# Optimization experiments

Hardware: AMD Instinct MI355X
Metric: run time of the kernel (lower is better)

## Reference

```python
import jax, jax.numpy as jnp
import numpy as np

# Conv config (matches init_kwargs): 3x3 conv, 256->256, stride 1, pad 1
KH, KW = 3, 3
STRIDE = (1, 1)
PAD = ((1, 1), (1, 1))


def setup_inputs() -> dict:
    key = jax.random.key(0)
    k1, k2, k3 = jax.random.split(key, 3)
    x = jax.random.normal(k1, (32, 256, 56, 56), dtype=jnp.float32)
    # linear.weight = conv.weight.view(C_out, C_in*kH*kW) -> [256, 2304]
    weight = jax.random.normal(k2, (256, 256 * KH * KW), dtype=jnp.float32) * 0.02
    bias = jax.random.normal(k3, (256,), dtype=jnp.float32)
    return {"x": x, "weight": weight, "bias": bias}


def reference(x, weight, bias):
    # im2col (same layout/order as F.unfold: feature dim = C * kH * kW, c-major)
    # patches: [N, C*kH*kW, H_out, W_out]
    patches = jax.lax.conv_general_dilated_patches(
        x, filter_shape=(KH, KW), window_strides=STRIDE, padding=PAD
    )
    # dense GEMM over the unfolded feature dim (the nn.Linear)
    y = jnp.einsum("nkhw,ok->nohw", patches, weight)
    y = y + bias[None, :, None, None]
    return y
```

## Files before the change

kernel.cpp:

```cpp
#include <hip/hip_runtime.h>
#include <hip/hip_bf16.h>

typedef short bf16x8 __attribute__((ext_vector_type(8)));
typedef float f32x4  __attribute__((ext_vector_type(4)));
typedef unsigned int uint4v __attribute__((ext_vector_type(4)));

#define HWHW   3136
#define ROWSH  40
#define ROWBYTES 80

__device__ __forceinline__ unsigned short f2bf(float f) {
    unsigned int u = __float_as_uint(f);
    u += 0x7fffu + ((u >> 16) & 1u);
    return (unsigned short)(u >> 16);
}

__global__ void wprep(const float* __restrict__ w, unsigned short* __restrict__ wt) {
    int idx = blockIdx.x * blockDim.x + threadIdx.x;
    int e    = idx & 7;
    int lane = (idx >> 3) & 63;
    int om   = (idx >> 9) & 15;
    int c8   = (idx >> 13) & 7;
    int t    = idx >> 16;
    int o = om * 16 + (lane & 15);
    int c = c8 * 32 + (lane >> 4) * 8 + e;
    wt[idx] = f2bf(w[o * 2304 + c * 9 + t]);
}

__global__ void xprep(const float* __restrict__ x, unsigned short* __restrict__ xt) {
    const int hp = blockIdx.x;
    const int c8 = blockIdx.y;
    const int n  = blockIdx.z;
    const int t  = threadIdx.x;
    const int wp  = t >> 2;
    const int ccq = t & 3;
    const int h = hp - 1, w = wp - 1;
    const bool ok = (h >= 0) && (h < 56) && (w >= 0) && (w < 56);
    const int sp = ok ? (h * 56 + w) : 0;
    const float* xr = x + ((size_t)n * 256 + c8 * 32 + ccq * 8) * HWHW + sp;
    uint4v d;
#pragma unroll
    for (int p = 0; p < 4; ++p) {
        float f0 = ok ? xr[(size_t)(2 * p) * HWHW] : 0.0f;
        float f1 = ok ? xr[(size_t)(2 * p + 1) * HWHW] : 0.0f;
        d[p] = (unsigned)f2bf(f0) | ((unsigned)f2bf(f1) << 16);
    }
    *(uint4v*)(xt + ((((size_t)n * 8 + c8) * 58 + hp) * 2048) + wp * 32 + ccq * 8) = d;
}

__global__ __launch_bounds__(256, 2)
void conv_main(const unsigned short* __restrict__ xt, const unsigned short* __restrict__ wt,
               const float* __restrict__ bias, float* __restrict__ out) {
    __shared__ __align__(16) short xs[2][6 * 64 * ROWSH];

    const int bx = blockIdx.x;
    const int hb = bx >> 1;
    const int bm = bx & 1;
    const int n  = blockIdx.y;
    const int h0 = hb * 4;

    const int tid  = threadIdx.x;
    const int lane = tid & 63;
    const int wv   = tid >> 6;
    const int wm   = wv & 1;
    const int ng   = wv >> 1;
    const int g    = lane >> 4;
    const int lcol = lane & 15;

    int bboff[7][3];
#pragma unroll
    for (int f = 0; f < 7; ++f) {
        int j = ng * 112 + f * 16 + lcol;
        int r = j / 56, wc = j % 56;
#pragma unroll
        for (int kw = 0; kw < 3; ++kw) {
            int ww  = wc + kw;
            int bit = (ww >> 3) & 1;
            bboff[f][kw] = (r * 64 + ww) * ROWBYTES + 16 * (g ^ bit);
        }
    }

    const int sg  = tid & 3;
    const int swp = (tid >> 2) & 63;
    const int swb = swp * ROWBYTES + 16 * (sg ^ ((swp >> 3) & 1));

    const unsigned short* wl = wt + (size_t)lane * 8;
    const int obase = bm * 8 + wm * 4;

    f32x4 acc[4][7];
#pragma unroll
    for (int m = 0; m < 4; ++m)
#pragma unroll
        for (int f = 0; f < 7; ++f) acc[m][f] = (f32x4){0.f, 0.f, 0.f, 0.f};

    bf16x8 sv[6];
    auto s_load = [&](int c8) {
        const unsigned short* p = xt + (((size_t)n * 8 + c8) * 58 + h0) * 2048 + swp * 32 + sg * 8;
#pragma unroll
        for (int r = 0; r < 6; ++r) sv[r] = *(const bf16x8*)(p + (size_t)r * 2048);
    };
    auto s_write = [&](int buf) {
        char* d = (char*)&xs[buf][0] + swb;
#pragma unroll
        for (int r = 0; r < 6; ++r)
            *(bf16x8*)(d + r * 64 * ROWBYTES) = sv[r];
    };

    s_load(0);
    s_write(0);
    __syncthreads();

    for (int c8 = 0; c8 < 8; ++c8) {
        const bool more = c8 < 7;
        const char* xb = (const char*)&xs[c8 & 1][0];

        bf16x8 a0[4], a1[4];
#pragma unroll
        for (int m = 0; m < 4; ++m)
            a0[m] = *(const bf16x8*)(wl + (size_t)((c8 * 16) + obase + m) * 512);

#pragma unroll
        for (int t = 0; t < 9; ++t) {
            bf16x8* ac = (t & 1) ? a1 : a0;
            bf16x8* an = (t & 1) ? a0 : a1;
            if (t < 8) {
#pragma unroll
                for (int m = 0; m < 4; ++m)
                    an[m] = *(const bf16x8*)(wl + (size_t)((((t + 1) * 8 + c8) * 16) + obase + m) * 512);
            }
            const int kh = t / 3, kw = t % 3;
            const int dt = kh * 64 * ROWBYTES;
#pragma unroll
            for (int f = 0; f < 7; ++f) {
                bf16x8 b = *(const bf16x8*)(xb + bboff[f][kw] + dt);
#pragma unroll
                for (int m = 0; m < 4; ++m)
                    acc[m][f] = __builtin_amdgcn_mfma_f32_16x16x32_bf16(ac[m], b, acc[m][f], 0, 0, 0);
            }
            if (t == 4 && more) s_load(c8 + 1);
        }

        if (more) s_write((c8 + 1) & 1);
        __syncthreads();
    }

#pragma unroll
    for (int m = 0; m < 4; ++m) {
#pragma unroll
        for (int q = 0; q < 4; ++q) {
            int o = bm * 128 + wm * 64 + m * 16 + 4 * g + q;
            float bs = bias[o];
            float* yo = out + ((size_t)n * 256 + o) * HWHW + hb * 224;
#pragma unroll
            for (int f = 0; f < 7; ++f) {
                int j = ng * 112 + f * 16 + lcol;
                yo[j] = acc[m][f][q] + bs;
            }
        }
    }
}

__global__ __launch_bounds__(512, 2)
void conv_fallback(const float* __restrict__ x, const unsigned short* __restrict__ wt,
                   const float* __restrict__ bias, float* __restrict__ out) {
    __shared__ short xs[2][348 * 40];
    const int hb = blockIdx.x, n = blockIdx.y, h0 = hb * 4;
    const int tid = threadIdx.x, lane = tid & 63, wv = tid >> 6;
    const int wm = wv & 3, ng = wv >> 2, g = lane >> 4, lcol = lane & 15;
    int bbase[7];
#pragma unroll
    for (int f = 0; f < 7; ++f) {
        int j = ng * 112 + f * 16 + lcol;
        bbase[f] = ((j / 56) * 58 + (j % 56)) * 40 + 8 * g;
    }
    const int cpair = tid >> 5, col0 = tid & 31;
    const float* xn = x + (size_t)n * 256 * HWHW;
    float sv0[6][2], sv1[6][2];
    f32x4 acc[4][7];
#pragma unroll
    for (int m = 0; m < 4; ++m)
#pragma unroll
        for (int f = 0; f < 7; ++f) acc[m][f] = (f32x4){0.f, 0.f, 0.f, 0.f};
    const unsigned short* wl = wt + (size_t)lane * 8;
    auto stage_load = [&](int c8) {
        const float* xc0 = xn + (size_t)(c8 * 32 + 2 * cpair) * HWHW;
        const float* xc1 = xc0 + HWHW;
#pragma unroll
        for (int r = 0; r < 6; ++r) {
            int hh = h0 - 1 + r;
            bool rok = (hh >= 0) & (hh < 56);
#pragma unroll
            for (int ci = 0; ci < 2; ++ci) {
                int col = col0 + 32 * ci, ww = col - 1;
                bool ok = rok & (col < 58) & (ww >= 0) & (ww < 56);
                int off = hh * 56 + ww;
                sv0[r][ci] = ok ? xc0[off] : 0.0f;
                sv1[r][ci] = ok ? xc1[off] : 0.0f;
            }
        }
    };
    auto stage_write = [&](int buf) {
#pragma unroll
        for (int r = 0; r < 6; ++r)
#pragma unroll
            for (int ci = 0; ci < 2; ++ci) {
                int col = col0 + 32 * ci;
                if (col < 58) {
                    unsigned int p = (unsigned int)f2bf(sv0[r][ci]) |
                                     ((unsigned int)f2bf(sv1[r][ci]) << 16);
                    *(unsigned int*)&xs[buf][(r * 58 + col) * 40 + 2 * cpair] = p;
                }
            }
    };
    stage_load(0); stage_write(0);
    __syncthreads();
    for (int c8 = 0; c8 < 8; ++c8) {
        if (c8 < 7) stage_load(c8 + 1);
        const short* xb = &xs[c8 & 1][0];
        bf16x8 a0[4], a1[4];
#pragma unroll
        for (int m = 0; m < 4; ++m)
            a0[m] = *(const bf16x8*)(wl + (size_t)((c8 * 16) + 4 * wm + m) * 512);
#pragma unroll
        for (int t = 0; t < 9; ++t) {
            bf16x8* ac = (t & 1) ? a1 : a0;
            bf16x8* an = (t & 1) ? a0 : a1;
            if (t < 8) {
#pragma unroll
                for (int m = 0; m < 4; ++m)
                    an[m] = *(const bf16x8*)(wl + (size_t)((((t + 1) * 8 + c8) * 16) + 4 * wm + m) * 512);
            }
            const int dt = ((t / 3) * 58 + (t % 3)) * 40;
#pragma unroll
            for (int f = 0; f < 7; ++f) {
                bf16x8 b = *(const bf16x8*)&xb[bbase[f] + dt];
#pragma unroll
                for (int m = 0; m < 4; ++m)
                    acc[m][f] = __builtin_amdgcn_mfma_f32_16x16x32_bf16(ac[m], b, acc[m][f], 0, 0, 0);
            }
        }
        if (c8 < 7) stage_write((c8 + 1) & 1);
        __syncthreads();
    }
#pragma unroll
    for (int m = 0; m < 4; ++m) {
#pragma unroll
        for (int q = 0; q < 4; ++q) {
            int o = 64 * wm + 16 * m + 4 * g + q;
            float bs = bias[o];
            float* yo = out + ((size_t)n * 256 + o) * HWHW + h0 * 56;
#pragma unroll
            for (int f = 0; f < 7; ++f) {
                int j = ng * 112 + f * 16 + lcol;
                yo[j] = acc[m][f][q] + bs;
            }
        }
    }
}

extern "C" void kernel_launch(void* const* d_in, const int* in_sizes, int n_in,
                              void* d_out, int out_size, void* d_ws, size_t ws_size,
                              hipStream_t stream) {
    const float* x    = (const float*)d_in[0];
    const float* w    = (const float*)d_in[1];
    const float* bias = (const float*)d_in[2];
    float* out        = (float*)d_out;
    unsigned short* wt = (unsigned short*)d_ws;
    unsigned short* xtp = (unsigned short*)((char*)d_ws + 1179648);

    wprep<<<2304, 256, 0, stream>>>(w, wt);
    if (ws_size >= (size_t)1179648 + 60817408) {
        xprep<<<dim3(58, 8, 32), 256, 0, stream>>>(x, xtp);
        conv_main<<<dim3(28, 32), 256, 0, stream>>>(xtp, wt, bias, out);
    } else {
        conv_fallback<<<dim3(14, 32), 512, 0, stream>>>(x, wt, bias, out);
    }
}
```

Before: 147.2 us.

## Stage input tiles with direct global-to-LDS loads and swizzle block order

Replaces the register-staged copy of input tiles into shared memory with asynchronous global_load_lds transfers. It switches the padded 80-byte row layout to an unpadded 64-byte row with an XOR swizzle. Blocks now use a 1D grid whose index is remapped so neighbouring tiles spread across the chiplets, and the MFMA loop is wrapped in s_setprio. The aim is to cut VGPR pressure, shared-memory footprint and copy instructions, but prefetch now starts only at the last tap, which leaves less time to hide the global load latency before the barrier.

```diff
diff --git a/kernel.cpp b/kernel.cpp
--- a/kernel.cpp
+++ b/kernel.cpp
@@ -6,8 +6,6 @@
 typedef unsigned int uint4v __attribute__((ext_vector_type(4)));
 
 #define HWHW   3136
-#define ROWSH  40
-#define ROWBYTES 80
 
 __device__ __forceinline__ unsigned short f2bf(float f) {
     unsigned int u = __float_as_uint(f);
@@ -51,12 +49,14 @@
 __global__ __launch_bounds__(256, 2)
 void conv_main(const unsigned short* __restrict__ xt, const unsigned short* __restrict__ wt,
                const float* __restrict__ bias, float* __restrict__ out) {
-    __shared__ __align__(16) short xs[2][6 * 64 * ROWSH];
-
-    const int bx = blockIdx.x;
-    const int hb = bx >> 1;
-    const int bm = bx & 1;
-    const int n  = blockIdx.y;
+    __shared__ __align__(16) short xs[2][6 * 64 * 32];
+
+    const int bid  = blockIdx.x;
+    const int bid2 = (bid & 7) * 112 + (bid >> 3);
+    const int n  = bid2 / 28;
+    const int r2 = bid2 % 28;
+    const int hb = r2 >> 1;
+    const int bm = r2 & 1;
     const int h0 = hb * 4;
 
     const int tid  = threadIdx.x;
@@ -74,15 +74,10 @@
         int r = j / 56, wc = j % 56;
 #pragma unroll
         for (int kw = 0; kw < 3; ++kw) {
-            int ww  = wc + kw;
-            int bit = (ww >> 3) & 1;
-            bboff[f][kw] = (r * 64 + ww) * ROWBYTES + 16 * (g ^ bit);
-        }
-    }
-
-    const int sg  = tid & 3;
-    const int swp = (tid >> 2) & 63;
-    const int swb = swp * ROWBYTES + 16 * (sg ^ ((swp >> 3) & 1));
+            int ww = wc + kw;
+            bboff[f][kw] = ((r * 64 + ww) << 6) + 16 * (g ^ (ww & 3));
+        }
+    }
 
     const unsigned short* wl = wt + (size_t)lane * 8;
     const int obase = bm * 8 + wm * 4;
@@ -93,21 +88,30 @@
 #pragma unroll
         for (int f = 0; f < 7; ++f) acc[m][f] = (f32x4){0.f, 0.f, 0.f, 0.f};
 
-    bf16x8 sv[6];
-    auto s_load = [&](int c8) {
-        const unsigned short* p = xt + (((size_t)n * 8 + c8) * 58 + h0) * 2048 + swp * 32 + sg * 8;
-#pragma unroll
-        for (int r = 0; r < 6; ++r) sv[r] = *(const bf16x8*)(p + (size_t)r * 2048);
-    };
-    auto s_write = [&](int buf) {
-        char* d = (char*)&xs[buf][0] + swb;
-#pragma unroll
-        for (int r = 0; r < 6; ++r)
-            *(bf16x8*)(d + r * 64 * ROWBYTES) = sv[r];
-    };
-
-    s_load(0);
-    s_write(0);
+    const int s_ww0 = lane >> 2;
+    const int s_gg  = (lane & 3) ^ ((lane >> 2) & 3);
+    auto stage = [&](int c8, int buf) {
+#pragma unroll
+        for (int i = 0; i < 6; ++i) {
+            const int run = wv * 6 + i;
+            const int r   = run >> 2;
+            const int ww  = (run & 3) * 16 + s_ww0;
+            const unsigned short* src =
+                xt + (((size_t)n * 8 + c8) * 58 + h0 + r) * 2048 + ww * 32 + s_gg * 8;
+            __builtin_amdgcn_global_load_lds(
+                (const __attribute__((address_space(1))) unsigned int*)src,
+                (__attribute__((address_space(3))) unsigned int*)
+                    (((char*)&xs[buf][0]) + run * 1024),
+                16, 0, 0);
+        }
+    };
+    auto a_load = [&](bf16x8* dst, int c8, int t) {
+#pragma unroll
+        for (int m = 0; m < 4; ++m)
+            dst[m] = *(const bf16x8*)(wl + (size_t)((t * 8 + c8) * 16 + obase + m) * 512);
+    };
+
+    stage(0, 0);
     __syncthreads();
 
     for (int c8 = 0; c8 < 8; ++c8) {
@@ -115,21 +119,18 @@
         const char* xb = (const char*)&xs[c8 & 1][0];
 
         bf16x8 a0[4], a1[4];
-#pragma unroll
-        for (int m = 0; m < 4; ++m)
-            a0[m] = *(const bf16x8*)(wl + (size_t)((c8 * 16) + obase + m) * 512);
+        a_load(a0, c8, 0);
 
 #pragma unroll
         for (int t = 0; t < 9; ++t) {
             bf16x8* ac = (t & 1) ? a1 : a0;
             bf16x8* an = (t & 1) ? a0 : a1;
-            if (t < 8) {
-#pragma unroll
-                for (int m = 0; m < 4; ++m)
-                    an[m] = *(const bf16x8*)(wl + (size_t)((((t + 1) * 8 + c8) * 16) + obase + m) * 512);
-            }
+            if (t < 8) a_load(an, c8, t + 1);
+            else if (more) stage(c8 + 1, (c8 + 1) & 1);
+
             const int kh = t / 3, kw = t % 3;
-            const int dt = kh * 64 * ROWBYTES;
+            const int dt = kh * 4096;
+            __builtin_amdgcn_s_setprio(1);
 #pragma unroll
             for (int f = 0; f < 7; ++f) {
                 bf16x8 b = *(const bf16x8*)(xb + bboff[f][kw] + dt);
@@ -137,10 +138,8 @@
                 for (int m = 0; m < 4; ++m)
                     acc[m][f] = __builtin_amdgcn_mfma_f32_16x16x32_bf16(ac[m], b, acc[m][f], 0, 0, 0);
             }
-            if (t == 4 && more) s_load(c8 + 1);
-        }
-
-        if (more) s_write((c8 + 1) & 1);
+            __builtin_amdgcn_s_setprio(0);
+        }
         __syncthreads();
     }
 
@@ -271,7 +270,7 @@
     wprep<<<2304, 256, 0, stream>>>(w, wt);
     if (ws_size >= (size_t)1179648 + 60817408) {
         xprep<<<dim3(58, 8, 32), 256, 0, stream>>>(x, xtp);
-        conv_main<<<dim3(28, 32), 256, 0, stream>>>(xtp, wt, bias, out);
+        conv_main<<<896, 256, 0, stream>>>(xtp, wt, bias, out);
     } else {
         conv_fallback<<<dim3(14, 32), 512, 0, stream>>>(x, wt, bias, out);
     }
```

After: 134.2 us. 8.8% less time.
